# Kernel tuning notes

Measured on AMD Instinct MI355X. Metric: run time of the kernel, lower is better.

## Reference

```python
import jax, jax.numpy as jnp
import numpy as np

N_NODES = 100000
N_EDGES = 1600000
N_GRAPHS = 512
IN_CH = 64
HID = 64
OUT_CH = 2
NC = 3


def setup_inputs() -> dict:
    key = jax.random.key(0)
    ks = jax.random.split(key, 10)
    x = jax.random.normal(ks[0], (N_NODES, IN_CH), dtype=jnp.float32)
    edge_index = jax.random.randint(ks[1], (2, N_EDGES), 0, N_NODES, dtype=jnp.int64)
    batch = jnp.sort(jax.random.randint(ks[2], (N_NODES,), 0, N_GRAPHS, dtype=jnp.int64))
    s = 1.0 / np.sqrt(HID)
    W_rel = jax.random.normal(ks[3], (NC, HID, HID), dtype=jnp.float32) * s
    W_root = jax.random.normal(ks[4], (NC, HID, HID), dtype=jnp.float32) * s
    b_conv = jax.random.normal(ks[5], (NC, HID), dtype=jnp.float32) * s
    W1 = jax.random.normal(ks[6], (HID, 2 * HID), dtype=jnp.float32) * s
    b1 = jax.random.normal(ks[7], (2 * HID,), dtype=jnp.float32) * s
    W2 = jax.random.normal(ks[8], (2 * HID, OUT_CH), dtype=jnp.float32) * (1.0 / np.sqrt(2 * HID))
    b2 = jax.random.normal(ks[9], (OUT_CH,), dtype=jnp.float32) * (1.0 / np.sqrt(2 * HID))
    return {"x": x, "edge_index": edge_index, "batch": batch,
            "W_rel": W_rel, "W_root": W_root, "b_conv": b_conv,
            "W1": W1, "b1": b1, "W2": W2, "b2": b2}


def reference(x, edge_index, batch, W_rel, W_root, b_conv, W1, b1, W2, b2):
    src, dst = edge_index[0], edge_index[1]
    h = x
    for i in range(NC):
        # PyG GraphConv(aggr='add'): lin_rel(scatter_add(h[src] -> dst)) + lin_root(h)
        agg = jax.ops.segment_sum(h[src], dst, num_segments=N_NODES)  # [N, HID]
        h = jax.nn.relu(agg @ W_rel[i] + b_conv[i] + h @ W_root[i])
    pooled = jax.ops.segment_sum(h, batch, num_segments=N_GRAPHS)  # [G, HID]
    # MLP readout [HID, 2*HID, OUT]
    out = jax.nn.sigmoid(jax.nn.relu(pooled @ W1 + b1) @ W2 + b2)  # [G, OUT]
    return out, pooled
```

## Files before the change

kernel.cpp:

```cpp
#include <hip/hip_runtime.h>
#include <math.h>

#define N_NODES 100000
#define N_EDGES 1600000
#define N_GRAPHS 512
#define HID 64
#define NC 3

#define NBUCK 782
#define EPB 4096
#define NPBLK 391
#define PSTRIDE 3072
#define BSTRIDE 4096
#define DUMMY N_NODES

typedef unsigned int uint;

__device__ __forceinline__ ushort f2bf(float f) {
    uint u = __float_as_uint(f);
    u += 0x7fffu + ((u >> 16) & 1u);
    return (ushort)(u >> 16);
}
__device__ __forceinline__ uint packbf2(float a, float b) {
    return (uint)f2bf(a) | ((uint)f2bf(b) << 16);
}


__global__ __launch_bounds__(256) void partition_kernel(const int* __restrict__ src,
                                                        const int* __restrict__ dst,
                                                        int* __restrict__ ccursor,
                                                        int2* __restrict__ part) {
    __shared__ int cnt[NBUCK];
    __shared__ int base[NBUCK];
    __shared__ int cur[NBUCK];
    for (int i = threadIdx.x; i < NBUCK; i += 256) { cnt[i] = 0; cur[i] = 0; }
    __syncthreads();
    const int4* d4 = (const int4*)dst;
    const int4* s4 = (const int4*)src;
    int i0 = blockIdx.x * (EPB / 4);
    int i1 = min(i0 + EPB / 4, N_EDGES / 4);
    for (int i = i0 + threadIdx.x; i < i1; i += 256) {
        int4 d = d4[i];
        atomicAdd(&cnt[d.x >> 7], 1);
        atomicAdd(&cnt[d.y >> 7], 1);
        atomicAdd(&cnt[d.z >> 7], 1);
        atomicAdd(&cnt[d.w >> 7], 1);
    }
    __syncthreads();
    for (int i = threadIdx.x; i < NBUCK; i += 256)
        base[i] = cnt[i] ? (i * PSTRIDE + atomicAdd(&ccursor[i], cnt[i])) : 0;
    __syncthreads();
    for (int i = i0 + threadIdx.x; i < i1; i += 256) {
        int4 d = d4[i];
        int4 s = s4[i];
        int b0 = d.x >> 7; part[base[b0] + atomicAdd(&cur[b0], 1)] = make_int2(s.x, d.x);
        int b1 = d.y >> 7; part[base[b1] + atomicAdd(&cur[b1], 1)] = make_int2(s.y, d.y);
        int b2 = d.z >> 7; part[base[b2] + atomicAdd(&cur[b2], 1)] = make_int2(s.z, d.z);
        int b3 = d.w >> 7; part[base[b3] + atomicAdd(&cur[b3], 1)] = make_int2(s.w, d.w);
    }
}


__global__ __launch_bounds__(256) void bcsr_kernel(const int2* __restrict__ part,
                                                   const int* __restrict__ ccursor,
                                                   int* __restrict__ row_ptr,
                                                   int* __restrict__ pdeg,
                                                   int* __restrict__ col) {
    __shared__ int deg[128];
    __shared__ int cur[128];
    __shared__ int pre[128];
    __shared__ int ss[256];
    int b = blockIdx.x;
    int t = threadIdx.x;
    int s0 = b * PSTRIDE;
    int s1 = s0 + ccursor[b];
    if (t < 128) { deg[t] = 0; cur[t] = 0; }
    __syncthreads();
    for (int e = s0 + t; e < s1; e += 256)
        atomicAdd(&deg[part[e].y & 127], 1);
    __syncthreads();
    int v = (t < 128) ? ((deg[t] + 7) & ~7) : 0;
    int val = v;
    ss[t] = val;
    __syncthreads();
    for (int off = 1; off < 256; off <<= 1) {
        int o = (t >= off) ? ss[t - off] : 0;
        __syncthreads();
        val += o;
        ss[t] = val;
        __syncthreads();
    }
    if (t < 128) pre[t] = val - v;
    __syncthreads();
    int base = b * BSTRIDE;
    int node = b * 128 + t;
    if (t < 128 && node < N_NODES) {
        row_ptr[node] = base + pre[t];
        pdeg[node] = v;
    }
    for (int e = s0 + t; e < s1; e += 256) {
        int2 p = part[e];
        int nl = p.y & 127;
        int r = atomicAdd(&cur[nl], 1);
        col[base + pre[nl] + r] = p.x;
    }
    __syncthreads();
    if (t < 128) {
        for (int i = deg[t]; i < v; i++)
            col[base + pre[t] + i] = DUMMY;
    }
}


__global__ __launch_bounds__(256) void cvt_kernel(const float* __restrict__ x,
                                                  ushort* __restrict__ hX) {
    int i = blockIdx.x * blockDim.x + threadIdx.x;
    int stride = gridDim.x * blockDim.x;
    const float4* x4 = (const float4*)x;
    for (; i < N_NODES * HID / 4; i += stride) {
        float4 v = x4[i];
        uint2 o;
        o.x = packbf2(v.x, v.y);
        o.y = packbf2(v.z, v.w);
        *(uint2*)(hX + (size_t)i * 4) = o;
    }
}


__global__ __launch_bounds__(256) void wprep_kernel(const float* __restrict__ W_rel,
                                                    const float* __restrict__ W_root,
                                                    ushort* __restrict__ WT) {
    int i = blockIdx.x * blockDim.x + threadIdx.x;
    if (i >= NC * 2 * HID * HID) return;
    int l = i / (2 * HID * HID);
    int rem = i % (2 * HID * HID);
    int m = rem / (HID * HID);
    int j = rem % (HID * HID);
    int colc = j / HID;
    int k = j % HID;
    const float* W = (m ? W_root : W_rel) + l * HID * HID;
    WT[i] = f2bf(W[k * HID + colc]);
}


#define ACC4(A, v) { A.x += __uint_as_float((v).x << 16); \
                     A.y += __uint_as_float((v).x & 0xffff0000u); \
                     A.z += __uint_as_float((v).y << 16); \
                     A.w += __uint_as_float((v).y & 0xffff0000u); }

__global__ __launch_bounds__(256) void gather_kernel(
    const ushort* __restrict__ hin, ushort* __restrict__ agg,
    const int* __restrict__ row_ptr, const int* __restrict__ pdeg,
    const int* __restrict__ col)
{
    int lane = threadIdx.x & 63;
    int slot = lane >> 4;
    int ch   = (lane & 15) * 4;
    int gwid = (blockIdx.x * blockDim.x + threadIdx.x) >> 6;
    int nwaves = (gridDim.x * blockDim.x) >> 6;

    for (int n0 = gwid * 4; n0 < N_NODES; n0 += nwaves * 4) {
        int n = n0 + slot;
        const int* row = col + row_ptr[n];
        int pd = pdeg[n];
        float4 a0 = {0.f,0.f,0.f,0.f}, a1 = {0.f,0.f,0.f,0.f};
        float4 a2 = {0.f,0.f,0.f,0.f}, a3 = {0.f,0.f,0.f,0.f};
        for (int e = 0; e < pd; e += 8) {
            int4 ca = *(const int4*)(row + e);
            int4 cb = *(const int4*)(row + e + 4);
            uint2 v0 = *(const uint2*)(hin + (size_t)ca.x * HID + ch);
            uint2 v1 = *(const uint2*)(hin + (size_t)ca.y * HID + ch);
            uint2 v2 = *(const uint2*)(hin + (size_t)ca.z * HID + ch);
            uint2 v3 = *(const uint2*)(hin + (size_t)ca.w * HID + ch);
            uint2 v4 = *(const uint2*)(hin + (size_t)cb.x * HID + ch);
            uint2 v5 = *(const uint2*)(hin + (size_t)cb.y * HID + ch);
            uint2 v6 = *(const uint2*)(hin + (size_t)cb.z * HID + ch);
            uint2 v7 = *(const uint2*)(hin + (size_t)cb.w * HID + ch);
            ACC4(a0, v0); ACC4(a1, v1); ACC4(a2, v2); ACC4(a3, v3);
            ACC4(a0, v4); ACC4(a1, v5); ACC4(a2, v6); ACC4(a3, v7);
        }
        a0.x += a1.x + a2.x + a3.x;
        a0.y += a1.y + a2.y + a3.y;
        a0.z += a1.z + a2.z + a3.z;
        a0.w += a1.w + a2.w + a3.w;
        uint2 o;
        o.x = packbf2(a0.x, a0.y);
        o.y = packbf2(a0.z, a0.w);
        *(uint2*)(agg + (size_t)n * HID + ch) = o;
    }
}


__global__ __launch_bounds__(256) void transform_kernel(
    const ushort* __restrict__ hin, const ushort* __restrict__ agg,
    ushort* __restrict__ hout, const ushort* __restrict__ WTl,
    const float* __restrict__ bias)
{
    typedef __attribute__((ext_vector_type(8))) short short8;
    typedef __attribute__((ext_vector_type(4))) float f32x4;
    __shared__ float lds[4][16][68];
    int lane = threadIdx.x & 63;
    int wid  = threadIdx.x >> 6;
    int mrow = lane & 15;
    int kg   = lane >> 4;
    int gw = (blockIdx.x * blockDim.x + threadIdx.x) >> 6;
    int nw = (gridDim.x * blockDim.x) >> 6;

    short8 Bf[4][4];
#pragma unroll
    for (int c = 0; c < 4; c++)
#pragma unroll
        for (int m = 0; m < 2; m++)
#pragma unroll
            for (int h = 0; h < 2; h++)
                Bf[c][m * 2 + h] = *(const short8*)(
                    WTl + m * HID * HID + (c * 16 + mrow) * HID + h * 32 + kg * 8);

    float bv[4];
#pragma unroll
    for (int c = 0; c < 4; c++) bv[c] = bias[c * 16 + mrow];

    for (int ng = gw; ng < N_NODES / 16; ng += nw) {
        size_t rb = ((size_t)ng * 16 + mrow) * HID + kg * 8;
        short8 Ah0 = *(const short8*)(hin + rb);
        short8 Ah1 = *(const short8*)(hin + rb + 32);
        short8 Aa0 = *(const short8*)(agg + rb);
        short8 Aa1 = *(const short8*)(agg + rb + 32);
#pragma unroll
        for (int c = 0; c < 4; c++) {
            f32x4 acc = {0.f, 0.f, 0.f, 0.f};
            acc = __builtin_amdgcn_mfma_f32_16x16x32_bf16(Aa0, Bf[c][0], acc, 0, 0, 0);
            acc = __builtin_amdgcn_mfma_f32_16x16x32_bf16(Aa1, Bf[c][1], acc, 0, 0, 0);
            acc = __builtin_amdgcn_mfma_f32_16x16x32_bf16(Ah0, Bf[c][2], acc, 0, 0, 0);
            acc = __builtin_amdgcn_mfma_f32_16x16x32_bf16(Ah1, Bf[c][3], acc, 0, 0, 0);
#pragma unroll
            for (int r = 0; r < 4; r++)
                lds[wid][kg * 4 + r][c * 16 + mrow] = fmaxf(acc[r] + bv[c], 0.f);
        }
        asm volatile("s_waitcnt lgkmcnt(0)" ::: "memory");
        const float* lr = &lds[wid][mrow][kg * 16];
        float4 f0 = *(const float4*)(lr + 0);
        float4 f1 = *(const float4*)(lr + 4);
        float4 f2 = *(const float4*)(lr + 8);
        float4 f3 = *(const float4*)(lr + 12);
        uint4 o0, o1;
        o0.x = packbf2(f0.x, f0.y); o0.y = packbf2(f0.z, f0.w);
        o0.z = packbf2(f1.x, f1.y); o0.w = packbf2(f1.z, f1.w);
        o1.x = packbf2(f2.x, f2.y); o1.y = packbf2(f2.z, f2.w);
        o1.z = packbf2(f3.x, f3.y); o1.w = packbf2(f3.z, f3.w);
        ushort* orow = hout + ((size_t)ng * 16 + mrow) * HID + kg * 16;
        *(uint4*)(orow) = o0;
        *(uint4*)(orow + 8) = o1;
    }
}


__global__ __launch_bounds__(256) void pool_kernel(
    const ushort* __restrict__ h, const int* __restrict__ batch,
    float* __restrict__ pooled_ws) {
    const int CH = 64;
    int lane = threadIdx.x & 63;
    int gwid = (blockIdx.x * blockDim.x + threadIdx.x) >> 6;
    int n0 = gwid * CH;
    if (n0 >= N_NODES) return;
    int nend = min(n0 + CH, N_NODES);
    int cur = batch[n0];
    float acc = 0.f;
    for (int n = n0; n < nend; n++) {
        int g = batch[n];
        if (g != cur) {
            atomicAdd(&pooled_ws[cur * HID + lane], acc);
            acc = 0.f;
            cur = g;
        }
        acc += __uint_as_float(((uint)h[(size_t)n * HID + lane]) << 16);
    }
    atomicAdd(&pooled_ws[cur * HID + lane], acc);
}


__global__ void mlp_kernel(const float* __restrict__ pooled_ws,
                           const float* __restrict__ W1, const float* __restrict__ b1,
                           const float* __restrict__ W2, const float* __restrict__ b2,
                           float* __restrict__ out, float* __restrict__ pooled_out) {
    __shared__ float sp[HID];
    __shared__ float red[4];
    int g = blockIdx.x, t = threadIdx.x;
    if (t < HID) {
        float v = pooled_ws[g * HID + t];
        sp[t] = v;
        pooled_out[g * HID + t] = v;
    }
    __syncthreads();
    float acc = b1[t];
#pragma unroll
    for (int k = 0; k < HID; k++) acc = fmaf(sp[k], W1[k * 128 + t], acc);
    float hid = fmaxf(acc, 0.f);
    float p0 = hid * W2[t * 2 + 0];
    float p1 = hid * W2[t * 2 + 1];
    for (int off = 32; off > 0; off >>= 1) {
        p0 += __shfl_down(p0, off, 64);
        p1 += __shfl_down(p1, off, 64);
    }
    int wave = t >> 6, lane = t & 63;
    if (lane == 0) { red[wave * 2 + 0] = p0; red[wave * 2 + 1] = p1; }
    __syncthreads();
    if (t == 0) {
        float o0 = red[0] + red[2] + b2[0];
        float o1 = red[1] + red[3] + b2[1];
        out[g * 2 + 0] = 1.f / (1.f + expf(-o0));
        out[g * 2 + 1] = 1.f / (1.f + expf(-o1));
    }
}


extern "C" void kernel_launch(void* const* d_in, const int* in_sizes, int n_in,
                              void* d_out, int out_size, void* d_ws, size_t ws_size,
                              hipStream_t stream) {
    const float* x      = (const float*)d_in[0];
    const int*   ei     = (const int*)d_in[1];
    const int*   batch  = (const int*)d_in[2];
    const float* W_rel  = (const float*)d_in[3];
    const float* W_root = (const float*)d_in[4];
    const float* b_conv = (const float*)d_in[5];
    const float* W1     = (const float*)d_in[6];
    const float* b1     = (const float*)d_in[7];
    const float* W2     = (const float*)d_in[8];
    const float* b2     = (const float*)d_in[9];

    float* outp       = (float*)d_out;
    float* pooled_out = (float*)d_out + N_GRAPHS * 2;

    const size_t HROWS_B = ((size_t)(N_NODES + 1) * HID * 2 + 255) & ~(size_t)255;

    char* ws = (char*)d_ws;
    size_t off = 0;
    ushort* hX = (ushort*)(ws + off); off += HROWS_B;
    ushort* hA = (ushort*)(ws + off); off += HROWS_B;
    ushort* hB = (ushort*)(ws + off); off += HROWS_B;
    ushort* gg = (ushort*)(ws + off); off += ((size_t)N_NODES * HID * 2 + 255) & ~(size_t)255;
    ushort* WT = (ushort*)(ws + off); off += ((size_t)NC * 2 * HID * HID * 2 + 255) & ~(size_t)255;
    int2* part    = (int2*)(ws + off); off += (size_t)NBUCK * PSTRIDE * 8;
    int* colidx   = (int*)(ws + off); off += (size_t)NBUCK * BSTRIDE * 4;
    int* row_ptr  = (int*)(ws + off); off += (size_t)(N_NODES + 4) * 4;
    int* pdeg     = (int*)(ws + off); off += (size_t)(N_NODES + 4) * 4;
    int* ccursor  = (int*)(ws + off); off += (size_t)NBUCK * 4;
    float* pooled_ws = (float*)(ws + off); off += (size_t)N_GRAPHS * HID * 4;

    const int* esrc = ei;
    const int* edst = ei + N_EDGES;

    hipMemsetAsync(ccursor, 0, (size_t)NBUCK * 4, stream);
    hipMemsetAsync(pooled_ws, 0, (size_t)N_GRAPHS * HID * 4, stream);
    hipMemsetAsync(hX + (size_t)N_NODES * HID, 0, HID * 2, stream);
    hipMemsetAsync(hA + (size_t)N_NODES * HID, 0, HID * 2, stream);
    hipMemsetAsync(hB + (size_t)N_NODES * HID, 0, HID * 2, stream);

    cvt_kernel<<<2048, 256, 0, stream>>>(x, hX);
    wprep_kernel<<<(NC * 2 * HID * HID + 255) / 256, 256, 0, stream>>>(W_rel, W_root, WT);

    partition_kernel<<<NPBLK, 256, 0, stream>>>(esrc, edst, ccursor, part);
    bcsr_kernel<<<NBUCK, 256, 0, stream>>>(part, ccursor, row_ptr, pdeg, colidx);

    gather_kernel<<<2048, 256, 0, stream>>>(hX, gg, row_ptr, pdeg, colidx);
    transform_kernel<<<512, 256, 0, stream>>>(hX, gg, hA, WT + 0 * 2 * HID * HID, b_conv + 0 * HID);
    gather_kernel<<<2048, 256, 0, stream>>>(hA, gg, row_ptr, pdeg, colidx);
    transform_kernel<<<512, 256, 0, stream>>>(hA, gg, hB, WT + 1 * 2 * HID * HID, b_conv + 1 * HID);
    gather_kernel<<<2048, 256, 0, stream>>>(hB, gg, row_ptr, pdeg, colidx);
    transform_kernel<<<512, 256, 0, stream>>>(hB, gg, hA, WT + 2 * 2 * HID * HID, b_conv + 2 * HID);

    pool_kernel<<<391, 256, 0, stream>>>(hA, batch, pooled_ws);
    mlp_kernel<<<N_GRAPHS, 128, 0, stream>>>(pooled_ws, W1, b1, W2, b2, outp, pooled_out);
}
```

Baseline: 306.1 us.

## Pack partitioned edges into 32-bit words and fold dummy-row memsets into cvt

Partitioned edge entries are now packed into one 32-bit word (7-bit local dst, 17-bit src) instead of an int2, halving the partition buffer traffic written by partition_kernel and read by bcsr_kernel. The partition kernel now uses 512 threads and 8192 edges per block, so there are fewer blocks and fewer global ccursor atomics. The three small memsets that zero the dummy rows move into cvt_kernel, removing three stream operations. The packing assumes source indices stay below 2^17.

Result: faster. 290.5 us (-5.1%).

```diff
diff --git a/kernel.cpp b/kernel.cpp
--- a/kernel.cpp
+++ b/kernel.cpp
@@ -8,11 +8,12 @@
 #define NC 3
 
 #define NBUCK 782
-#define EPB 4096
-#define NPBLK 391
+#define EPB 8192
+#define NPBLK 196
 #define PSTRIDE 3072
 #define BSTRIDE 4096
 #define DUMMY N_NODES
+#define SRCMASK 0x1FFFF
 
 typedef unsigned int uint;
 
@@ -26,20 +27,20 @@
 }
 
 
-__global__ __launch_bounds__(256) void partition_kernel(const int* __restrict__ src,
+__global__ __launch_bounds__(512) void partition_kernel(const int* __restrict__ src,
                                                         const int* __restrict__ dst,
                                                         int* __restrict__ ccursor,
-                                                        int2* __restrict__ part) {
+                                                        uint* __restrict__ part) {
     __shared__ int cnt[NBUCK];
     __shared__ int base[NBUCK];
     __shared__ int cur[NBUCK];
-    for (int i = threadIdx.x; i < NBUCK; i += 256) { cnt[i] = 0; cur[i] = 0; }
+    for (int i = threadIdx.x; i < NBUCK; i += 512) { cnt[i] = 0; cur[i] = 0; }
     __syncthreads();
     const int4* d4 = (const int4*)dst;
     const int4* s4 = (const int4*)src;
     int i0 = blockIdx.x * (EPB / 4);
     int i1 = min(i0 + EPB / 4, N_EDGES / 4);
-    for (int i = i0 + threadIdx.x; i < i1; i += 256) {
+    for (int i = i0 + threadIdx.x; i < i1; i += 512) {
         int4 d = d4[i];
         atomicAdd(&cnt[d.x >> 7], 1);
         atomicAdd(&cnt[d.y >> 7], 1);
@@ -47,21 +48,21 @@
         atomicAdd(&cnt[d.w >> 7], 1);
     }
     __syncthreads();
-    for (int i = threadIdx.x; i < NBUCK; i += 256)
+    for (int i = threadIdx.x; i < NBUCK; i += 512)
         base[i] = cnt[i] ? (i * PSTRIDE + atomicAdd(&ccursor[i], cnt[i])) : 0;
     __syncthreads();
-    for (int i = i0 + threadIdx.x; i < i1; i += 256) {
+    for (int i = i0 + threadIdx.x; i < i1; i += 512) {
         int4 d = d4[i];
         int4 s = s4[i];
-        int b0 = d.x >> 7; part[base[b0] + atomicAdd(&cur[b0], 1)] = make_int2(s.x, d.x);
-        int b1 = d.y >> 7; part[base[b1] + atomicAdd(&cur[b1], 1)] = make_int2(s.y, d.y);
-        int b2 = d.z >> 7; part[base[b2] + atomicAdd(&cur[b2], 1)] = make_int2(s.z, d.z);
-        int b3 = d.w >> 7; part[base[b3] + atomicAdd(&cur[b3], 1)] = make_int2(s.w, d.w);
-    }
-}
-
-
-__global__ __launch_bounds__(256) void bcsr_kernel(const int2* __restrict__ part,
+        int b0 = d.x >> 7; part[base[b0] + atomicAdd(&cur[b0], 1)] = ((uint)(d.x & 127) << 17) | (uint)s.x;
+        int b1 = d.y >> 7; part[base[b1] + atomicAdd(&cur[b1], 1)] = ((uint)(d.y & 127) << 17) | (uint)s.y;
+        int b2 = d.z >> 7; part[base[b2] + atomicAdd(&cur[b2], 1)] = ((uint)(d.z & 127) << 17) | (uint)s.z;
+        int b3 = d.w >> 7; part[base[b3] + atomicAdd(&cur[b3], 1)] = ((uint)(d.w & 127) << 17) | (uint)s.w;
+    }
+}
+
+
+__global__ __launch_bounds__(256) void bcsr_kernel(const uint* __restrict__ part,
                                                    const int* __restrict__ ccursor,
                                                    int* __restrict__ row_ptr,
                                                    int* __restrict__ pdeg,
@@ -77,7 +78,7 @@
     if (t < 128) { deg[t] = 0; cur[t] = 0; }
     __syncthreads();
     for (int e = s0 + t; e < s1; e += 256)
-        atomicAdd(&deg[part[e].y & 127], 1);
+        atomicAdd(&deg[part[e] >> 17], 1);
     __syncthreads();
     int v = (t < 128) ? ((deg[t] + 7) & ~7) : 0;
     int val = v;
@@ -99,10 +100,10 @@
         pdeg[node] = v;
     }
     for (int e = s0 + t; e < s1; e += 256) {
-        int2 p = part[e];
-        int nl = p.y & 127;
+        uint p = part[e];
+        int nl = p >> 17;
         int r = atomicAdd(&cur[nl], 1);
-        col[base + pre[nl] + r] = p.x;
+        col[base + pre[nl] + r] = (int)(p & SRCMASK);
     }
     __syncthreads();
     if (t < 128) {
@@ -113,7 +114,14 @@
 
 
 __global__ __launch_bounds__(256) void cvt_kernel(const float* __restrict__ x,
-                                                  ushort* __restrict__ hX) {
+                                                  ushort* __restrict__ hX,
+                                                  ushort* __restrict__ hA,
+                                                  ushort* __restrict__ hB) {
+    if (blockIdx.x == 0 && threadIdx.x < HID) {
+        hX[(size_t)N_NODES * HID + threadIdx.x] = 0;
+        hA[(size_t)N_NODES * HID + threadIdx.x] = 0;
+        hB[(size_t)N_NODES * HID + threadIdx.x] = 0;
+    }
     int i = blockIdx.x * blockDim.x + threadIdx.x;
     int stride = gridDim.x * blockDim.x;
     const float4* x4 = (const float4*)x;
@@ -340,7 +348,7 @@
     ushort* hB = (ushort*)(ws + off); off += HROWS_B;
     ushort* gg = (ushort*)(ws + off); off += ((size_t)N_NODES * HID * 2 + 255) & ~(size_t)255;
     ushort* WT = (ushort*)(ws + off); off += ((size_t)NC * 2 * HID * HID * 2 + 255) & ~(size_t)255;
-    int2* part    = (int2*)(ws + off); off += (size_t)NBUCK * PSTRIDE * 8;
+    uint* part    = (uint*)(ws + off); off += (size_t)NBUCK * PSTRIDE * 4;
     int* colidx   = (int*)(ws + off); off += (size_t)NBUCK * BSTRIDE * 4;
     int* row_ptr  = (int*)(ws + off); off += (size_t)(N_NODES + 4) * 4;
     int* pdeg     = (int*)(ws + off); off += (size_t)(N_NODES + 4) * 4;
@@ -352,14 +360,11 @@
 
     hipMemsetAsync(ccursor, 0, (size_t)NBUCK * 4, stream);
     hipMemsetAsync(pooled_ws, 0, (size_t)N_GRAPHS * HID * 4, stream);
-    hipMemsetAsync(hX + (size_t)N_NODES * HID, 0, HID * 2, stream);
-    hipMemsetAsync(hA + (size_t)N_NODES * HID, 0, HID * 2, stream);
-    hipMemsetAsync(hB + (size_t)N_NODES * HID, 0, HID * 2, stream);
-
-    cvt_kernel<<<2048, 256, 0, stream>>>(x, hX);
+
+    cvt_kernel<<<2048, 256, 0, stream>>>(x, hX, hA, hB);
     wprep_kernel<<<(NC * 2 * HID * HID + 255) / 256, 256, 0, stream>>>(W_rel, W_root, WT);
 
-    partition_kernel<<<NPBLK, 256, 0, stream>>>(esrc, edst, ccursor, part);
+    partition_kernel<<<NPBLK, 512, 0, stream>>>(esrc, edst, ccursor, part);
     bcsr_kernel<<<NBUCK, 256, 0, stream>>>(part, ccursor, row_ptr, pdeg, colidx);
 
     gather_kernel<<<2048, 256, 0, stream>>>(hX, gg, row_ptr, pdeg, colidx);
```
